# Kernel tuning notes

Measured on AMD Instinct MI355X. Metric: run time of the kernel, lower is better.

Reference implementation:

```python
import jax, jax.numpy as jnp
import numpy as np

TEMPERATURE = 0.07
HARD_K = 5


def setup_inputs() -> dict:
    key = jax.random.key(0)
    k1, k2 = jax.random.split(key)
    B, D = 8192, 512
    return {
        "v_emb": jax.random.normal(k1, (B, D), dtype=jnp.float32),
        "a_emb": jax.random.normal(k2, (B, D), dtype=jnp.float32),
    }


def _l2_normalize(x, eps=1e-12):
    # matches F.normalize(dim=1): x / max(||x||, eps)
    n = jnp.sqrt(jnp.sum(x * x, axis=1, keepdims=True))
    return x / jnp.maximum(n, eps)


def _one_direction(sim):
    # sim: [B, B]
    B = sim.shape[0]
    pos = jnp.diagonal(sim)  # [B]
    # exclude diagonal by pushing it to -inf, then top-k over remaining B-1 negatives
    neg = jnp.where(jnp.eye(B, dtype=bool), -jnp.inf, sim)
    k = min(HARD_K, B - 1)
    hard_neg, _ = jax.lax.top_k(neg, k)  # [B, k]
    logits = jnp.concatenate([pos[:, None], hard_neg], axis=1)  # [B, 1+k]
    # cross-entropy with label 0: mean(logsumexp(logits) - logits[:, 0])
    return jnp.mean(jax.nn.logsumexp(logits, axis=1) - logits[:, 0])


def reference(v_emb, a_emb):
    v = _l2_normalize(v_emb)
    a = _l2_normalize(a_emb)
    sim = (v @ a.T) / TEMPERATURE  # [B, B]
    loss_v2a = _one_direction(sim)
    loss_a2v = _one_direction(sim.T)
    return 0.5 * (loss_v2a + loss_a2v)
```

## Files before the change

### kernel.cpp

```cpp
#include <hip/hip_runtime.h>
#include <cstdint>
#include <cstddef>


#define TSCALE (1.0f/0.07f)
#define NEG_INF (-__builtin_inff())
#define KD 512
#define NB 8192
#define THR 0.115f
#define CAP 128
#define FBCAP 256

typedef __bf16 bf16_t;
typedef __bf16 bf16x8 __attribute__((ext_vector_type(8)));
typedef float  f32x4  __attribute__((ext_vector_type(4)));

#define TRY5(v, A0,A1,A2,A3,A4) do { float _v=(v); \
  if (_v > A4) { \
    if (_v > A2) { \
      if (_v > A0)      { A4=A3; A3=A2; A2=A1; A1=A0; A0=_v; } \
      else if (_v > A1) { A4=A3; A3=A2; A2=A1; A1=_v; } \
      else              { A4=A3; A3=A2; A2=_v; } \
    } else { \
      if (_v > A3)      { A4=A3; A3=_v; } \
      else              { A4=_v; } \
    } \
  } } while(0)

static __device__ __forceinline__ void load_lds16(const void* g, void* l) {
  __builtin_amdgcn_global_load_lds(
      (const __attribute__((address_space(1))) void*)g,
      (__attribute__((address_space(3))) void*)(uint32_t)(uintptr_t)l,
      16, 0, 0);
}

__global__ __launch_bounds__(256)
void nrm_kernel(const float* __restrict__ v, const float* __restrict__ a,
                bf16_t* __restrict__ vb, bf16_t* __restrict__ ab,
                float* __restrict__ pos)
{
  int row  = blockIdx.x * 4 + (threadIdx.x >> 6);
  int lane = threadIdx.x & 63;
  size_t base = (size_t)row * 512 + (size_t)lane * 8;
  float4 v0 = *(const float4*)(v + base);
  float4 v1 = *(const float4*)(v + base + 4);
  float4 a0 = *(const float4*)(a + base);
  float4 a1 = *(const float4*)(a + base + 4);

  float sv = v0.x*v0.x+v0.y*v0.y+v0.z*v0.z+v0.w*v0.w
           + v1.x*v1.x+v1.y*v1.y+v1.z*v1.z+v1.w*v1.w;
  float sa = a0.x*a0.x+a0.y*a0.y+a0.z*a0.z+a0.w*a0.w
           + a1.x*a1.x+a1.y*a1.y+a1.z*a1.z+a1.w*a1.w;
  float sd = v0.x*a0.x+v0.y*a0.y+v0.z*a0.z+v0.w*a0.w
           + v1.x*a1.x+v1.y*a1.y+v1.z*a1.z+v1.w*a1.w;
  #pragma unroll
  for (int m = 32; m; m >>= 1) {
    sv += __shfl_xor(sv, m);
    sa += __shfl_xor(sa, m);
    sd += __shfl_xor(sd, m);
  }
  float iv = 1.0f / fmaxf(sqrtf(sv), 1e-12f);
  float ia = 1.0f / fmaxf(sqrtf(sa), 1e-12f);

  bf16x8 ov, oa;
  ov[0]=(bf16_t)(v0.x*iv); ov[1]=(bf16_t)(v0.y*iv); ov[2]=(bf16_t)(v0.z*iv); ov[3]=(bf16_t)(v0.w*iv);
  ov[4]=(bf16_t)(v1.x*iv); ov[5]=(bf16_t)(v1.y*iv); ov[6]=(bf16_t)(v1.z*iv); ov[7]=(bf16_t)(v1.w*iv);
  oa[0]=(bf16_t)(a0.x*ia); oa[1]=(bf16_t)(a0.y*ia); oa[2]=(bf16_t)(a0.z*ia); oa[3]=(bf16_t)(a0.w*ia);
  oa[4]=(bf16_t)(a1.x*ia); oa[5]=(bf16_t)(a1.y*ia); oa[6]=(bf16_t)(a1.z*ia); oa[7]=(bf16_t)(a1.w*ia);
  *(bf16x8*)(vb + base) = ov;
  *(bf16x8*)(ab + base) = oa;
  if (lane == 0) pos[row] = sd * iv * ia * TSCALE;
}

__global__ __launch_bounds__(256, 5)
void gemm_topk(const bf16_t* __restrict__ vb, const bf16_t* __restrict__ ab,
               float* __restrict__ cand, unsigned int* __restrict__ cnt)
{
  __shared__ __align__(16) char lds[32768];
  int tid  = threadIdx.x;
  int wave = tid >> 6;
  int lane = tid & 63;
  int wr = wave >> 1, wc = wave & 1;
  int r = lane & 15, q = lane >> 4;

  int x     = blockIdx.x & 7;
  int local = blockIdx.x >> 3;
  int tr = (x >> 1) * 16 + (local >> 5);
  int tc = (x & 1) * 32 + (local & 31);
  int R0 = tr << 7, C0 = tc << 7;

  f32x4 acc[4][4];
  #pragma unroll
  for (int mi = 0; mi < 4; ++mi)
    #pragma unroll
    for (int ni = 0; ni < 4; ++ni)
      acc[mi][ni] = (f32x4){0.f,0.f,0.f,0.f};

  auto stage = [&](int k0, int buf) {
    #pragma unroll
    for (int call = 0; call < 2; ++call) {
      int p   = (call*4 + wave)*64 + lane;
      int row = p >> 2;
      int sl  = (p & 3) ^ (row & 3);
      const bf16_t* ga = vb + (size_t)(R0 + row)*KD + k0 + sl*8;
      const bf16_t* gb = ab + (size_t)(C0 + row)*KD + k0 + sl*8;
      char* la = lds + buf*16384 +        (call*4 + wave)*1024;
      char* lb = lds + buf*16384 + 8192 + (call*4 + wave)*1024;
      load_lds16(ga, la);
      load_lds16(gb, lb);
    }
  };

  stage(0, 0);
  __syncthreads();
  #pragma unroll
  for (int ks = 0; ks < 16; ++ks) {
    int cur = ks & 1;
    if (ks < 15) stage((ks+1)*32, cur ^ 1);
    const char* Ab = lds + cur*16384;
    const char* Bb = Ab + 8192;
    int ko = ((q ^ (r & 3)) << 4);
    bf16x8 af[4], bfr[4];
    #pragma unroll
    for (int mi = 0; mi < 4; ++mi)
      af[mi] = *(const bf16x8*)(Ab + (wr*64 + mi*16 + r)*64 + ko);
    #pragma unroll
    for (int ni = 0; ni < 4; ++ni)
      bfr[ni] = *(const bf16x8*)(Bb + (wc*64 + ni*16 + r)*64 + ko);
    #pragma unroll
    for (int mi = 0; mi < 4; ++mi)
      #pragma unroll
      for (int ni = 0; ni < 4; ++ni)
        acc[mi][ni] = __builtin_amdgcn_mfma_f32_16x16x32_bf16(af[mi], bfr[ni], acc[mi][ni], 0, 0, 0);
    __syncthreads();
  }

  if (tr == tc && wr == wc && (r >> 2) == q) {
    #pragma unroll
    for (int mi = 0; mi < 4; ++mi)
      acc[mi][mi][r & 3] = NEG_INF;
  }

  #pragma unroll
  for (int mi = 0; mi < 4; ++mi)
    #pragma unroll
    for (int ni = 0; ni < 4; ++ni) {
      f32x4 vq = acc[mi][ni];
      float m4 = fmaxf(fmaxf(vq[0], vq[1]), fmaxf(vq[2], vq[3]));
      if (m4 > THR) {
        int colg = C0 + wc*64 + ni*16 + r;
        #pragma unroll
        for (int rg = 0; rg < 4; ++rg) {
          float vv = vq[rg];
          if (vv > THR) {
            int rowg = R0 + wr*64 + mi*16 + q*4 + rg;
            unsigned int s1 = atomicAdd(&cnt[rowg], 1u);
            if (s1 < CAP) cand[(size_t)rowg*CAP + s1] = vv;
            unsigned int s2 = atomicAdd(&cnt[NB + colg], 1u);
            if (s2 < CAP) cand[(size_t)(NB + colg)*CAP + s2] = vv;
          }
        }
      }
    }
}

__global__ __launch_bounds__(256)
void merge_kernel(const float* __restrict__ cand, const unsigned int* __restrict__ cnt,
                  const float* __restrict__ pos, unsigned int* __restrict__ fbCnt,
                  unsigned int* __restrict__ fbList, float* __restrict__ loss)
{
  int obj = blockIdx.x*256 + threadIdx.x;
  int idx = obj & (NB-1);
  float p = pos[idx];
  unsigned int c = cnt[obj];
  if (c >= 5 && c <= CAP) {
    const float* s = cand + (size_t)obj*CAP;
    float a0=NEG_INF,a1=NEG_INF,a2=NEG_INF,a3=NEG_INF,a4=NEG_INF;
    for (unsigned int j = 0; j < c; ++j) TRY5(s[j], a0,a1,a2,a3,a4);
    float m = fmaxf(p, a0*TSCALE);
    float sum = expf(p - m)
              + expf(a0*TSCALE - m) + expf(a1*TSCALE - m) + expf(a2*TSCALE - m)
              + expf(a3*TSCALE - m) + expf(a4*TSCALE - m);
    loss[obj] = m + logf(sum) - p;
  } else {
    unsigned int slot = atomicAdd(fbCnt, 1u);
    if (slot < FBCAP) fbList[slot] = (unsigned int)obj;
    loss[obj] = 0.f;
  }
}

__global__ __launch_bounds__(256)
void fallback_kernel(const bf16_t* __restrict__ vb, const bf16_t* __restrict__ ab,
                     const float* __restrict__ pos,
                     const unsigned int* __restrict__ fbCnt,
                     const unsigned int* __restrict__ fbList,
                     float* __restrict__ loss)
{
  __shared__ float xrow[512];
  __shared__ float t5[256*5];
  unsigned int n = *fbCnt;
  if (n > FBCAP) n = FBCAP;
  for (unsigned int i = blockIdx.x; i < n; i += gridDim.x) {
    unsigned int obj = fbList[i];
    int dir = obj >> 13;
    int idx = obj & (NB-1);
    const bf16_t* X = dir ? ab : vb;
    const bf16_t* Y = dir ? vb : ab;
    __syncthreads();
    for (int j = threadIdx.x; j < 512; j += 256)
      xrow[j] = (float)X[(size_t)idx*KD + j];
    __syncthreads();
    float a0=NEG_INF,a1=NEG_INF,a2=NEG_INF,a3=NEG_INF,a4=NEG_INF;
    for (int cc = 0; cc < 32; ++cc) {
      int cidx = cc*256 + threadIdx.x;
      if (cidx == idx) continue;
      float d = 0.f;
      for (int k = 0; k < 512; k += 8) {
        bf16x8 y = *(const bf16x8*)(Y + (size_t)cidx*KD + k);
        #pragma unroll
        for (int e = 0; e < 8; ++e) d += xrow[k+e] * (float)y[e];
      }
      TRY5(d, a0,a1,a2,a3,a4);
    }
    float* dst = t5 + (size_t)threadIdx.x*5;
    dst[0]=a0; dst[1]=a1; dst[2]=a2; dst[3]=a3; dst[4]=a4;
    __syncthreads();
    if (threadIdx.x == 0) {
      float m0=NEG_INF,m1=NEG_INF,m2=NEG_INF,m3=NEG_INF,m4=NEG_INF;
      for (int j = 0; j < 256*5; ++j) TRY5(t5[j], m0,m1,m2,m3,m4);
      float p = pos[idx];
      float m = fmaxf(p, m0*TSCALE);
      float sum = expf(p - m)
                + expf(m0*TSCALE - m) + expf(m1*TSCALE - m) + expf(m2*TSCALE - m)
                + expf(m3*TSCALE - m) + expf(m4*TSCALE - m);
      loss[obj] = m + logf(sum) - p;
    }
    __syncthreads();
  }
}

__global__ __launch_bounds__(1024)
void final_kernel(const float* __restrict__ loss, float* __restrict__ out)
{
  int tid = threadIdx.x;
  float v = 0.f;
  #pragma unroll
  for (int j = 0; j < 16; ++j) v += loss[j*1024 + tid];
  #pragma unroll
  for (int m = 32; m; m >>= 1) v += __shfl_xor(v, m);
  __shared__ float wsum[16];
  if ((tid & 63) == 0) wsum[tid >> 6] = v;
  __syncthreads();
  if (tid == 0) {
    float t = 0.f;
    #pragma unroll
    for (int j = 0; j < 16; ++j) t += wsum[j];
    out[0] = 0.5f * t / 8192.0f;
  }
}

extern "C" void kernel_launch(void* const* d_in, const int* in_sizes, int n_in,
                              void* d_out, int out_size, void* d_ws, size_t ws_size,
                              hipStream_t stream)
{
  const float* v = (const float*)d_in[0];
  const float* a = (const float*)d_in[1];
  char* ws = (char*)d_ws;

  constexpr size_t OFF_AB   = 8ull*1024*1024;
  constexpr size_t OFF_POS  = 16ull*1024*1024;
  constexpr size_t OFF_CNT  = OFF_POS + 64*1024;
  constexpr size_t OFF_FBC  = OFF_CNT + 64*1024;
  constexpr size_t OFF_FBL  = OFF_FBC + 256;
  constexpr size_t OFF_LOSS = OFF_FBL + 4*1024;
  constexpr size_t OFF_CAND = 24ull*1024*1024;
  constexpr size_t ZERO_BYTES = OFF_FBL + 4*1024 - OFF_CNT;

  bf16_t* vb   = (bf16_t*)ws;
  bf16_t* ab   = (bf16_t*)(ws + OFF_AB);
  float* pos   = (float*)(ws + OFF_POS);
  unsigned int* cnt    = (unsigned int*)(ws + OFF_CNT);
  unsigned int* fbCnt  = (unsigned int*)(ws + OFF_FBC);
  unsigned int* fbList = (unsigned int*)(ws + OFF_FBL);
  float* loss  = (float*)(ws + OFF_LOSS);
  float* cand  = (float*)(ws + OFF_CAND);
  float* out   = (float*)d_out;

  hipMemsetAsync(ws + OFF_CNT, 0, ZERO_BYTES, stream);
  hipLaunchKernelGGL(nrm_kernel,      dim3(2048), dim3(256),  0, stream, v, a, vb, ab, pos);
  hipLaunchKernelGGL(gemm_topk,       dim3(4096), dim3(256),  0, stream, vb, ab, cand, cnt);
  hipLaunchKernelGGL(merge_kernel,    dim3(64),   dim3(256),  0, stream, cand, cnt, pos, fbCnt, fbList, loss);
  hipLaunchKernelGGL(fallback_kernel, dim3(64),   dim3(256),  0, stream, vb, ab, pos, fbCnt, fbList, loss);
  hipLaunchKernelGGL(final_kernel,    dim3(1),    dim3(1024), 0, stream, loss, out);
}
```

Measured before the change: 263.6 us.

## Replace global atomic candidate lists with per-tile LDS-counted slot buffers

Candidate counting in the GEMM epilogue now uses LDS atomics on per-tile row and column counters instead of global atomics on per-row counters. Each tile writes up to 6 candidates per row or column into its own slot region and stores a byte count. The merge kernel then walks all 64 tile partitions per object, and routes any overflow to the larger fallback list. This is meant to remove global atomic contention and the large memset, at the cost of more candidate storage, a longer merge scan and lower occupancy from launch bounds dropping from 5 to 4.

New measurement: 550.4 us. 2.09x slower.

```diff
diff --git a/kernel.cpp b/kernel.cpp
--- a/kernel.cpp
+++ b/kernel.cpp
@@ -8,8 +8,8 @@
 #define KD 512
 #define NB 8192
 #define THR 0.115f
-#define CAP 128
-#define FBCAP 256
+#define SLOTS 6
+#define FBCAP 16384
 
 typedef __bf16 bf16_t;
 typedef __bf16 bf16x8 __attribute__((ext_vector_type(8)));
@@ -72,9 +72,10 @@
   if (lane == 0) pos[row] = sd * iv * ia * TSCALE;
 }
 
-__global__ __launch_bounds__(256, 5)
+__global__ __launch_bounds__(256, 4)
 void gemm_topk(const bf16_t* __restrict__ vb, const bf16_t* __restrict__ ab,
-               float* __restrict__ cand, unsigned int* __restrict__ cnt)
+               float* __restrict__ candR, float* __restrict__ candC,
+               unsigned char* __restrict__ cntR, unsigned char* __restrict__ cntC)
 {
   __shared__ __align__(16) char lds[32768];
   int tid  = threadIdx.x;
@@ -141,6 +142,11 @@
       acc[mi][mi][r & 3] = NEG_INF;
   }
 
+  unsigned int* rc = (unsigned int*)lds;
+  unsigned int* cc = rc + 128;
+  if (tid < 256) rc[tid] = 0;
+  __syncthreads();
+
   #pragma unroll
   for (int mi = 0; mi < 4; ++mi)
     #pragma unroll
@@ -148,35 +154,52 @@
       f32x4 vq = acc[mi][ni];
       float m4 = fmaxf(fmaxf(vq[0], vq[1]), fmaxf(vq[2], vq[3]));
       if (m4 > THR) {
-        int colg = C0 + wc*64 + ni*16 + r;
+        int cl = wc*64 + ni*16 + r;
         #pragma unroll
         for (int rg = 0; rg < 4; ++rg) {
           float vv = vq[rg];
           if (vv > THR) {
-            int rowg = R0 + wr*64 + mi*16 + q*4 + rg;
-            unsigned int s1 = atomicAdd(&cnt[rowg], 1u);
-            if (s1 < CAP) cand[(size_t)rowg*CAP + s1] = vv;
-            unsigned int s2 = atomicAdd(&cnt[NB + colg], 1u);
-            if (s2 < CAP) cand[(size_t)(NB + colg)*CAP + s2] = vv;
+            int rl = wr*64 + mi*16 + q*4 + rg;
+            unsigned int s1 = atomicAdd(&rc[rl], 1u);
+            if (s1 < SLOTS) candR[((size_t)tc*NB + R0 + rl)*SLOTS + s1] = vv;
+            unsigned int s2 = atomicAdd(&cc[cl], 1u);
+            if (s2 < SLOTS) candC[((size_t)tr*NB + C0 + cl)*SLOTS + s2] = vv;
           }
         }
       }
     }
+  __syncthreads();
+
+  if (tid < 128)
+    cntR[(size_t)tc*NB + R0 + tid] = (unsigned char)min(rc[tid], 255u);
+  else
+    cntC[(size_t)tr*NB + C0 + (tid - 128)] = (unsigned char)min(cc[tid - 128], 255u);
 }
 
 __global__ __launch_bounds__(256)
-void merge_kernel(const float* __restrict__ cand, const unsigned int* __restrict__ cnt,
+void merge_kernel(const float* __restrict__ candR, const float* __restrict__ candC,
+                  const unsigned char* __restrict__ cntR, const unsigned char* __restrict__ cntC,
                   const float* __restrict__ pos, unsigned int* __restrict__ fbCnt,
                   unsigned int* __restrict__ fbList, float* __restrict__ loss)
 {
   int obj = blockIdx.x*256 + threadIdx.x;
+  int isCol = obj >> 13;
   int idx = obj & (NB-1);
+  const unsigned char* cnt = isCol ? cntC : cntR;
+  const float* cand = isCol ? candC : candR;
   float p = pos[idx];
-  unsigned int c = cnt[obj];
-  if (c >= 5 && c <= CAP) {
-    const float* s = cand + (size_t)obj*CAP;
-    float a0=NEG_INF,a1=NEG_INF,a2=NEG_INF,a3=NEG_INF,a4=NEG_INF;
+
+  float a0=NEG_INF,a1=NEG_INF,a2=NEG_INF,a3=NEG_INF,a4=NEG_INF;
+  int total = 0;
+  bool bad = false;
+  for (int t = 0; t < 64; ++t) {
+    unsigned int c = cnt[(size_t)t*NB + idx];
+    total += c;
+    if (c > SLOTS) { bad = true; continue; }
+    const float* s = cand + ((size_t)t*NB + idx)*SLOTS;
     for (unsigned int j = 0; j < c; ++j) TRY5(s[j], a0,a1,a2,a3,a4);
+  }
+  if (!bad && total >= 5) {
     float m = fmaxf(p, a0*TSCALE);
     float sum = expf(p - m)
               + expf(a0*TSCALE - m) + expf(a1*TSCALE - m) + expf(a2*TSCALE - m)
@@ -211,8 +234,8 @@
       xrow[j] = (float)X[(size_t)idx*KD + j];
     __syncthreads();
     float a0=NEG_INF,a1=NEG_INF,a2=NEG_INF,a3=NEG_INF,a4=NEG_INF;
-    for (int cc = 0; cc < 32; ++cc) {
-      int cidx = cc*256 + threadIdx.x;
+    for (int cc2 = 0; cc2 < 32; ++cc2) {
+      int cidx = cc2*256 + threadIdx.x;
       if (cidx == idx) continue;
       float d = 0.f;
       for (int k = 0; k < 512; k += 8) {
@@ -269,27 +292,30 @@
 
   constexpr size_t OFF_AB   = 8ull*1024*1024;
   constexpr size_t OFF_POS  = 16ull*1024*1024;
-  constexpr size_t OFF_CNT  = OFF_POS + 64*1024;
-  constexpr size_t OFF_FBC  = OFF_CNT + 64*1024;
+  constexpr size_t OFF_CNTR = OFF_POS + 64*1024;
+  constexpr size_t OFF_CNTC = OFF_CNTR + 512*1024;
+  constexpr size_t OFF_FBC  = OFF_CNTC + 512*1024;
   constexpr size_t OFF_FBL  = OFF_FBC + 256;
-  constexpr size_t OFF_LOSS = OFF_FBL + 4*1024;
-  constexpr size_t OFF_CAND = 24ull*1024*1024;
-  constexpr size_t ZERO_BYTES = OFF_FBL + 4*1024 - OFF_CNT;
+  constexpr size_t OFF_LOSS = OFF_FBL + 64*1024;
+  constexpr size_t OFF_CR   = 24ull*1024*1024;
+  constexpr size_t OFF_CC   = 40ull*1024*1024;
 
   bf16_t* vb   = (bf16_t*)ws;
   bf16_t* ab   = (bf16_t*)(ws + OFF_AB);
   float* pos   = (float*)(ws + OFF_POS);
-  unsigned int* cnt    = (unsigned int*)(ws + OFF_CNT);
+  unsigned char* cntR = (unsigned char*)(ws + OFF_CNTR);
+  unsigned char* cntC = (unsigned char*)(ws + OFF_CNTC);
   unsigned int* fbCnt  = (unsigned int*)(ws + OFF_FBC);
   unsigned int* fbList = (unsigned int*)(ws + OFF_FBL);
   float* loss  = (float*)(ws + OFF_LOSS);
-  float* cand  = (float*)(ws + OFF_CAND);
+  float* candR = (float*)(ws + OFF_CR);
+  float* candC = (float*)(ws + OFF_CC);
   float* out   = (float*)d_out;
 
-  hipMemsetAsync(ws + OFF_CNT, 0, ZERO_BYTES, stream);
+  hipMemsetAsync(ws + OFF_FBC, 0, 256, stream);
   hipLaunchKernelGGL(nrm_kernel,      dim3(2048), dim3(256),  0, stream, v, a, vb, ab, pos);
-  hipLaunchKernelGGL(gemm_topk,       dim3(4096), dim3(256),  0, stream, vb, ab, cand, cnt);
-  hipLaunchKernelGGL(merge_kernel,    dim3(64),   dim3(256),  0, stream, cand, cnt, pos, fbCnt, fbList, loss);
+  hipLaunchKernelGGL(gemm_topk,       dim3(4096), dim3(256),  0, stream, vb, ab, candR, candC, cntR, cntC);
+  hipLaunchKernelGGL(merge_kernel,    dim3(64),   dim3(256),  0, stream, candR, candC, cntR, cntC, pos, fbCnt, fbList, loss);
   hipLaunchKernelGGL(fallback_kernel, dim3(64),   dim3(256),  0, stream, vb, ab, pos, fbCnt, fbList, loss);
   hipLaunchKernelGGL(final_kernel,    dim3(1),    dim3(1024), 0, stream, loss, out);
 }
```
